# Kernel optimization log

Measured on AMD Instinct MI355X. Metric: run time of the kernel, lower is better.

## Reference

```python
import jax, jax.numpy as jnp
import numpy as np

B, F = 512, 512
K, D = 32, 16  # num_kernels, dim_per_kernel


def setup_inputs() -> dict:
    key = jax.random.key(0)
    kx, kt = jax.random.split(key)
    x = jax.random.normal(kx, (B, F), dtype=jnp.float32)
    # keras 'uniform' init is small-range uniform; scale similarly
    T = jax.random.uniform(kt, (F, K * D), dtype=jnp.float32, minval=-0.05, maxval=0.05)
    return {"x": x, "T": T}


def reference(x, T):
    # m: [B, K, D]
    m = (x @ T).reshape(-1, K, D)
    # all-pairs L1 distance per kernel: [B, B, K]
    abs_diffs = jnp.sum(jnp.abs(m[:, None, :, :] - m[None, :, :, :]), axis=-1)
    # minibatch features: sum_j exp(-||m_i - m_j||_1) -> [B, K]
    feats = jnp.sum(jnp.exp(-abs_diffs), axis=1)
    return jnp.concatenate([x, feats], axis=1)
```

## Files before the change

### kernel.cpp

```cpp
#include <hip/hip_runtime.h>
#include <hip/hip_bf16.h>
#include <math.h>

#define BSZ 512
#define FDIM 512
#define NK 32
#define DD 16
#define NDIM (NK*DD)
#define OUTW (FDIM + NK)

typedef __attribute__((ext_vector_type(8))) short short8;
typedef __attribute__((ext_vector_type(4))) float float4v;

static __device__ __forceinline__ unsigned short f2bfu(float f) {
  return __builtin_bit_cast(unsigned short, __float2bfloat16(f));
}

__global__ __launch_bounds__(256) void k_prep(
    const float* __restrict__ x, const float* __restrict__ T,
    unsigned short* __restrict__ xbf, unsigned short* __restrict__ tbf,
    float* __restrict__ out) {
  const int t = threadIdx.x, b = blockIdx.x;
  if (b < 64) {
    __shared__ unsigned short lt[64][65];
    const int tr = b >> 3, tc = b & 7;
    const float4* T4 = (const float4*)T;
#pragma unroll
    for (int qi = 0; qi < 4; ++qi) {
      const int idx = qi * 256 + t;
      const int rr = idx >> 4, c4 = idx & 15;
      const float4 v = T4[(size_t)(tr * 64 + rr) * 128 + tc * 16 + c4];
      lt[c4 * 4 + 0][rr] = f2bfu(v.x);
      lt[c4 * 4 + 1][rr] = f2bfu(v.y);
      lt[c4 * 4 + 2][rr] = f2bfu(v.z);
      lt[c4 * 4 + 3][rr] = f2bfu(v.w);
    }
    __syncthreads();
#pragma unroll
    for (int qi = 0; qi < 8; ++qi) {
      const int idx = qi * 256 + t;
      const int cl = idx >> 5, sg = idx & 31;
      ushort2 p;
      p.x = lt[cl][sg * 2];
      p.y = lt[cl][sg * 2 + 1];
      *(ushort2*)(tbf + (size_t)(tc * 64 + cl) * 512 + tr * 64 + sg * 2) = p;
    }
  } else {
    const int bb = b - 64;
    const float4* x4 = (const float4*)x;
#pragma unroll
    for (int qi = 0; qi < 4; ++qi) {
      const int i = bb * 1024 + qi * 256 + t;
      const float4 v = x4[i];
      const int orow = i >> 7, c4 = i & 127;
      *(float4*)(out + (size_t)orow * OUTW + c4 * 4) = v;
      ushort4 u;
      u.x = f2bfu(v.x); u.y = f2bfu(v.y); u.z = f2bfu(v.z); u.w = f2bfu(v.w);
      *(ushort4*)(xbf + (size_t)i * 4) = u;
    }
    const int idx2 = bb * 256 + t;
    out[(size_t)(idx2 >> 5) * OUTW + FDIM + (idx2 & 31)] = 0.f;
  }
}

__global__ __launch_bounds__(256, 4) void k_gemm(
    const unsigned short* __restrict__ xbf,
    const unsigned short* __restrict__ tbf, float* __restrict__ m) {
  const int t  = threadIdx.x;
  const int b  = blockIdx.x;
  const int rg = b >> 5, cg = b & 31;
  const int r0 = rg * 16, c0 = cg * 16;
  const int lane = t & 63;
  const int w    = __builtin_amdgcn_readfirstlane(t >> 6);
  const int mi   = lane & 15;
  const int q    = lane >> 4;

  const unsigned short* __restrict__ xa =
      xbf + (size_t)(r0 + mi) * FDIM + 128 * w + 8 * q;
  const unsigned short* __restrict__ tb =
      tbf + (size_t)(c0 + mi) * FDIM + 128 * w + 8 * q;

  short8 af[4], bf[4];
#pragma unroll
  for (int j = 0; j < 4; ++j) {
    af[j] = *(const short8*)(xa + 32 * j);
    bf[j] = *(const short8*)(tb + 32 * j);
  }
  float4v acc = {0.f, 0.f, 0.f, 0.f};
#pragma unroll
  for (int j = 0; j < 4; ++j)
    acc = __builtin_amdgcn_mfma_f32_16x16x32_bf16(af[j], bf[j], acc, 0, 0, 0);

  __shared__ float red[4][16][16];
#pragma unroll
  for (int r = 0; r < 4; ++r) red[w][q * 4 + r][mi] = acc[r];
  __syncthreads();
  {
    const int orow = t >> 4, ocol = t & 15;
    const float s = red[0][orow][ocol] + red[1][orow][ocol] +
                    red[2][orow][ocol] + red[3][orow][ocol];
    m[(size_t)(r0 + orow) * NDIM + c0 + ocol] = s;
  }
}

__global__ __launch_bounds__(256) void k_dist(
    const float* __restrict__ m, float* __restrict__ out) {
  __shared__ float Bs[128 * DD];
  __shared__ float red[256];
  const int t   = threadIdx.x;
  const int bid = blockIdx.x;
  const int ig  = bid >> 7;
  const int k   = (bid >> 2) & 31;
  const int jq  = bid & 3;
  const int lane = t & 63;
  const int i    = ig * 64 + lane;

  const float4* ap = (const float4*)(m + (size_t)i * NDIM + k * DD);
  const float4 A0 = ap[0], A1 = ap[1], A2 = ap[2], A3 = ap[3];

  const float* mb = m + (size_t)(jq * 128) * NDIM + k * DD;
#pragma unroll
  for (int qq = 0; qq < 2; ++qq) {
    const int idx = qq * 256 + t;
    const int jrow = idx >> 2, part = idx & 3;
    *(float4*)&Bs[jrow * DD + part * 4] =
        *(const float4*)(mb + (size_t)jrow * NDIM + part * 4);
  }
  __syncthreads();

  float a[DD];
  a[0]=A0.x; a[1]=A0.y; a[2]=A0.z;  a[3]=A0.w;
  a[4]=A1.x; a[5]=A1.y; a[6]=A1.z;  a[7]=A1.w;
  a[8]=A2.x; a[9]=A2.y; a[10]=A2.z; a[11]=A2.w;
  a[12]=A3.x;a[13]=A3.y;a[14]=A3.z; a[15]=A3.w;

  const int w = __builtin_amdgcn_readfirstlane(t >> 6);
  const int jbase = w * 32;
  float f = 0.f;
#pragma unroll 4
  for (int j = 0; j < 32; ++j) {
    const float4* bp = (const float4*)&Bs[(jbase + j) * DD];
    const float4 b0 = bp[0], b1 = bp[1], b2 = bp[2], b3 = bp[3];
    float d =
        fabsf(a[0]  - b0.x) + fabsf(a[1]  - b0.y) +
        fabsf(a[2]  - b0.z) + fabsf(a[3]  - b0.w) +
        fabsf(a[4]  - b1.x) + fabsf(a[5]  - b1.y) +
        fabsf(a[6]  - b1.z) + fabsf(a[7]  - b1.w) +
        fabsf(a[8]  - b2.x) + fabsf(a[9]  - b2.y) +
        fabsf(a[10] - b2.z) + fabsf(a[11] - b2.w) +
        fabsf(a[12] - b3.x) + fabsf(a[13] - b3.y) +
        fabsf(a[14] - b3.z) + fabsf(a[15] - b3.w);
    f += __expf(-d);
  }

  red[t] = f;
  __syncthreads();
  if (t < 64) {
    const float s = red[t] + red[t + 64] + red[t + 128] + red[t + 192];
    atomicAdd(out + (size_t)(ig * 64 + t) * OUTW + FDIM + k, s);
  }
}

extern "C" void kernel_launch(void* const* d_in, const int* in_sizes, int n_in,
                              void* d_out, int out_size, void* d_ws,
                              size_t ws_size, hipStream_t stream) {
  (void)in_sizes; (void)n_in; (void)out_size; (void)ws_size;
  const float* x = (const float*)d_in[0];
  const float* T = (const float*)d_in[1];
  float* out = (float*)d_out;
  float* m = (float*)d_ws;
  unsigned short* xbf = (unsigned short*)((char*)d_ws + (size_t)BSZ * NDIM * 4);
  unsigned short* tbf = xbf + (size_t)BSZ * FDIM;

  hipLaunchKernelGGL(k_prep, dim3(128), dim3(256), 0, stream,
                     x, T, xbf, tbf, out);
  hipLaunchKernelGGL(k_gemm, dim3(1024), dim3(256), 0, stream, xbf, tbf, m);
  hipLaunchKernelGGL(k_dist, dim3(1024), dim3(256), 0, stream, m, out);
}
```

Measured before the change: 74.25 us.

## Register-tile k_dist as 4x4 i-j blocks with 64x64 tiles and more blocks

Restructures the pairwise L1-distance kernel so each thread computes a 4x4 block of (i,j) distances, with both A and B rows staged in shared memory as 64-row tiles. Each loaded B vector is reused across four A rows, which cuts LDS traffic per FLOP. The grid doubles to 2048 blocks with 8 j-tiles per (i-group, k). Partial sums are reduced via shuffles plus a small shared buffer before the atomics. The trade-off is higher register pressure (64 A values plus accumulators) and twice as many atomicAdds into the output.

```diff
diff --git a/kernel.cpp b/kernel.cpp
--- a/kernel.cpp
+++ b/kernel.cpp
@@ -103,60 +103,83 @@
   }
 }
 
-__global__ __launch_bounds__(256) void k_dist(
+__global__ __launch_bounds__(256, 4) void k_dist(
     const float* __restrict__ m, float* __restrict__ out) {
-  __shared__ float Bs[128 * DD];
-  __shared__ float red[256];
+  __shared__ float As[64 * DD];
+  __shared__ float Bs[64 * DD];
+  __shared__ float red[4][4][16];
   const int t   = threadIdx.x;
   const int bid = blockIdx.x;
-  const int ig  = bid >> 7;
-  const int k   = (bid >> 2) & 31;
-  const int jq  = bid & 3;
+  const int ig  = bid >> 8;
+  const int k   = (bid >> 3) & 31;
+  const int jo  = bid & 7;
   const int lane = t & 63;
-  const int i    = ig * 64 + lane;
-
-  const float4* ap = (const float4*)(m + (size_t)i * NDIM + k * DD);
-  const float4 A0 = ap[0], A1 = ap[1], A2 = ap[2], A3 = ap[3];
-
-  const float* mb = m + (size_t)(jq * 128) * NDIM + k * DD;
-#pragma unroll
-  for (int qq = 0; qq < 2; ++qq) {
-    const int idx = qq * 256 + t;
-    const int jrow = idx >> 2, part = idx & 3;
-    *(float4*)&Bs[jrow * DD + part * 4] =
-        *(const float4*)(mb + (size_t)jrow * NDIM + part * 4);
+  const int w    = t >> 6;
+
+  {
+    const int row = t >> 2, part = t & 3;
+    *(float4*)&As[row * DD + part * 4] = *(const float4*)(
+        m + (size_t)(ig * 64 + row) * NDIM + k * DD + part * 4);
+    *(float4*)&Bs[row * DD + part * 4] = *(const float4*)(
+        m + (size_t)(jo * 64 + row) * NDIM + k * DD + part * 4);
   }
   __syncthreads();
 
-  float a[DD];
-  a[0]=A0.x; a[1]=A0.y; a[2]=A0.z;  a[3]=A0.w;
-  a[4]=A1.x; a[5]=A1.y; a[6]=A1.z;  a[7]=A1.w;
-  a[8]=A2.x; a[9]=A2.y; a[10]=A2.z; a[11]=A2.w;
-  a[12]=A3.x;a[13]=A3.y;a[14]=A3.z; a[15]=A3.w;
-
-  const int w = __builtin_amdgcn_readfirstlane(t >> 6);
-  const int jbase = w * 32;
-  float f = 0.f;
-#pragma unroll 4
-  for (int j = 0; j < 32; ++j) {
-    const float4* bp = (const float4*)&Bs[(jbase + j) * DD];
+  const int it = lane & 15;
+  const int jt = (lane >> 4) + 4 * w;
+
+  float a4[4][DD];
+#pragma unroll
+  for (int ii = 0; ii < 4; ++ii) {
+    const float4* ap = (const float4*)&As[(it * 4 + ii) * DD];
+#pragma unroll
+    for (int p = 0; p < 4; ++p) {
+      const float4 v = ap[p];
+      a4[ii][p * 4 + 0] = v.x; a4[ii][p * 4 + 1] = v.y;
+      a4[ii][p * 4 + 2] = v.z; a4[ii][p * 4 + 3] = v.w;
+    }
+  }
+
+  float dist[4][4];
+#pragma unroll
+  for (int ii = 0; ii < 4; ++ii)
+#pragma unroll
+    for (int jj = 0; jj < 4; ++jj) dist[ii][jj] = 0.f;
+
+#pragma unroll
+  for (int jj = 0; jj < 4; ++jj) {
+    const float4* bp = (const float4*)&Bs[(jt * 4 + jj) * DD];
     const float4 b0 = bp[0], b1 = bp[1], b2 = bp[2], b3 = bp[3];
-    float d =
-        fabsf(a[0]  - b0.x) + fabsf(a[1]  - b0.y) +
-        fabsf(a[2]  - b0.z) + fabsf(a[3]  - b0.w) +
-        fabsf(a[4]  - b1.x) + fabsf(a[5]  - b1.y) +
-        fabsf(a[6]  - b1.z) + fabsf(a[7]  - b1.w) +
-        fabsf(a[8]  - b2.x) + fabsf(a[9]  - b2.y) +
-        fabsf(a[10] - b2.z) + fabsf(a[11] - b2.w) +
-        fabsf(a[12] - b3.x) + fabsf(a[13] - b3.y) +
-        fabsf(a[14] - b3.z) + fabsf(a[15] - b3.w);
-    f += __expf(-d);
-  }
-
-  red[t] = f;
+    float bb[DD];
+    bb[0]=b0.x; bb[1]=b0.y; bb[2]=b0.z;  bb[3]=b0.w;
+    bb[4]=b1.x; bb[5]=b1.y; bb[6]=b1.z;  bb[7]=b1.w;
+    bb[8]=b2.x; bb[9]=b2.y; bb[10]=b2.z; bb[11]=b2.w;
+    bb[12]=b3.x;bb[13]=b3.y;bb[14]=b3.z; bb[15]=b3.w;
+#pragma unroll
+    for (int ii = 0; ii < 4; ++ii) {
+      float d = 0.f;
+#pragma unroll
+      for (int dd = 0; dd < DD; ++dd) d += fabsf(a4[ii][dd] - bb[dd]);
+      dist[ii][jj] = d;
+    }
+  }
+
+  float f4[4];
+#pragma unroll
+  for (int ii = 0; ii < 4; ++ii) {
+    f4[ii] = __expf(-dist[ii][0]) + __expf(-dist[ii][1]) +
+             __expf(-dist[ii][2]) + __expf(-dist[ii][3]);
+    f4[ii] += __shfl_xor(f4[ii], 16);
+    f4[ii] += __shfl_xor(f4[ii], 32);
+  }
+  if (lane < 16) {
+#pragma unroll
+    for (int ii = 0; ii < 4; ++ii) red[w][ii][lane] = f4[ii];
+  }
   __syncthreads();
   if (t < 64) {
-    const float s = red[t] + red[t + 64] + red[t + 128] + red[t + 192];
+    const float s = red[0][t & 3][t >> 2] + red[1][t & 3][t >> 2] +
+                    red[2][t & 3][t >> 2] + red[3][t & 3][t >> 2];
     atomicAdd(out + (size_t)(ig * 64 + t) * OUTW + FDIM + k, s);
   }
 }
@@ -175,5 +198,5 @@
   hipLaunchKernelGGL(k_prep, dim3(128), dim3(256), 0, stream,
                      x, T, xbf, tbf, out);
   hipLaunchKernelGGL(k_gemm, dim3(1024), dim3(256), 0, stream, xbf, tbf, m);
-  hipLaunchKernelGGL(k_dist, dim3(1024), dim3(256), 0, stream, m, out);
-}
+  hipLaunchKernelGGL(k_dist, dim3(2048), dim3(256), 0, stream, m, out);
+}
```

Result: slower. 87.78 us (+18.2%).
